# Optimization experiments

Measured on AMD Instinct MI355X. Metric: run time of the kernel, lower is better.

## Reference

```python
import jax, jax.numpy as jnp
import numpy as np

N0, N1, N2, N3 = 600000, 100000, 20000, 4096
E0, E1, E2 = 1500000, 200000, 40960
D_IN, D_H, D_OUT = 100, 256, 47


def setup_inputs() -> dict:
    key = jax.random.key(0)
    ks = jax.random.split(key, 16)
    inp = {
        "x": jax.random.normal(ks[0], (N0, D_IN), jnp.float32),
        "ei0_src": jax.random.randint(ks[1], (E0,), 0, N0, jnp.int32),
        "ei0_dst": jax.random.randint(ks[2], (E0,), 0, N1, jnp.int32),
        "ei1_src": jax.random.randint(ks[3], (E1,), 0, N1, jnp.int32),
        "ei1_dst": jax.random.randint(ks[4], (E1,), 0, N2, jnp.int32),
        "ei2_src": jax.random.randint(ks[5], (E2,), 0, N2, jnp.int32),
        "ei2_dst": jax.random.randint(ks[6], (E2,), 0, N3, jnp.int32),
        "Wl0": jax.random.normal(ks[7], (D_IN, D_H), jnp.float32) * 0.1,
        "Wr0": jax.random.normal(ks[8], (D_IN, D_H), jnp.float32) * 0.1,
        "b0": jnp.zeros((D_H,), jnp.float32),
        "Wl1": jax.random.normal(ks[9], (D_H, D_H), jnp.float32) * 0.06,
        "Wr1": jax.random.normal(ks[10], (D_H, D_H), jnp.float32) * 0.06,
        "b1": jnp.zeros((D_H,), jnp.float32),
        "Wl2": jax.random.normal(ks[11], (D_H, D_OUT), jnp.float32) * 0.06,
        "Wr2": jax.random.normal(ks[12], (D_H, D_OUT), jnp.float32) * 0.06,
        "b2": jnp.zeros((D_OUT,), jnp.float32),
    }
    return inp


def _sage_layer(x_src, x_tgt, src, dst, n_tgt, Wl, Wr, b):
    # PyG SAGEConv (mean aggr): out = lin_l(mean_{j in N(i)} x_j) + lin_r(x_i)
    msgs = x_src[src]                                   # [E, d] gather
    s = jax.ops.segment_sum(msgs, dst, num_segments=n_tgt)
    cnt = jax.ops.segment_sum(jnp.ones((src.shape[0],), x_src.dtype), dst,
                              num_segments=n_tgt)[:, None]
    mean = s / jnp.maximum(cnt, 1.0)
    return mean @ Wl + x_tgt @ Wr + b


def reference(x, ei0_src, ei0_dst, ei1_src, ei1_dst, ei2_src, ei2_dst,
              Wl0, Wr0, b0, Wl1, Wr1, b1, Wl2, Wr2, b2):
    h = _sage_layer(x, x[:N1], ei0_src, ei0_dst, N1, Wl0, Wr0, b0)
    h = jax.nn.relu(h)  # dropout is identity in eval mode
    h = _sage_layer(h, h[:N2], ei1_src, ei1_dst, N2, Wl1, Wr1, b1)
    h = jax.nn.relu(h)
    h = _sage_layer(h, h[:N3], ei2_src, ei2_dst, N3, Wl2, Wr2, b2)
    return jax.nn.log_softmax(h, axis=-1)
```

## Files before the change

kernel.cpp:

```cpp
#include <hip/hip_runtime.h>

#define NN0 600000
#define NN1 100000
#define NN2 20000
#define NN3 4096
#define EE0 1500000
#define EE1 200000
#define EE2 40960
#define DIN 100
#define DH  256
#define DOUT 47
#define NTOT (NN1 + NN2 + NN3)

#define RNG 16384
#define CH0 32768
#define NC0 46
#define R0  7
#define CH1 16384
#define NC1 13
#define R1  2
#define CH2 8192
#define NC2 5
#define R2  1
#define HL0 (NC0 * R0)
#define HL1 (NC1 * R1)
#define HL2 (NC2 * R2)
#define HLT (HL0 + HL1 + HL2)
#define NGMAX 46

#define NB0 98
#define NB1 20
#define NB2 4
#define NBT 122

#define HB0 5860
#define HB1 782
#define HB2 160
#define HBE (HB0 + HB1 + HB2)
#define PACKBLK 108
#define CONVBLK 3072

typedef unsigned int uint;
typedef unsigned short ushort;
typedef __attribute__((ext_vector_type(8))) short bhalf8;
typedef __attribute__((ext_vector_type(4))) float f32x4;

union U16B {
    uint2  u2[2];
    uint4  u4;
    bhalf8 s8;
    ushort us[8];
};

__device__ __forceinline__ ushort f2bf(float f) {
    uint u = __float_as_uint(f);
    uint r = (u + 0x7FFFu + ((u >> 16) & 1u)) >> 16;
    return (ushort)r;
}
__device__ __forceinline__ float bf2f(uint bits16) {
    return __uint_as_float(bits16 << 16);
}

__global__ __launch_bounds__(256)
void hist_lds(const int* __restrict__ e0d, const int* __restrict__ e1d,
              const int* __restrict__ e2d, int* __restrict__ cntp,
              int* __restrict__ pos0, int* __restrict__ pos1,
              int* __restrict__ pos2) {
    __shared__ int lcnt[RNG];
    int b = blockIdx.x, tid = threadIdx.x;
    const int* dstp; int E, CH, c, r, nbase, layerN;
    int* pos;
    if (b < HL0) {
        dstp = e0d; E = EE0; CH = CH0; c = b / R0; r = b % R0;
        nbase = 0; layerN = NN1; pos = pos0;
    } else if (b < HL0 + HL1) {
        int bb = b - HL0;
        dstp = e1d; E = EE1; CH = CH1; c = bb / R1; r = bb % R1;
        nbase = NN1; layerN = NN2; pos = pos1;
    } else {
        int bb = b - HL0 - HL1;
        dstp = e2d; E = EE2; CH = CH2; c = bb; r = 0;
        nbase = NN1 + NN2; layerN = NN3; pos = pos2;
    }
    for (int i = tid; i < RNG; i += 256) lcnt[i] = 0;
    __syncthreads();
    int rbase = r * RNG;
    long long ebase = (long long)c * CH;
    for (int i = tid; i < CH; i += 256) {
        int e = (int)(ebase + i);
        if (e < E) {
            int d = dstp[e];
            unsigned li = (unsigned)(d - rbase);
            if (li < RNG) pos[e] = atomicAdd(&lcnt[li], 1);
        }
    }
    __syncthreads();
    for (int i = tid; i < RNG; i += 256) {
        int node = rbase + i;
        if (node < layerN)
            cntp[(size_t)c * NTOT + nbase + node] = lcnt[i];
    }
}

__device__ __forceinline__ void pack_one(const float* B, int K, int N, int NB,
                                         ushort* out, int bid, int l) {
    int kstep = bid / NB;
    int c = bid % NB;
    U16B v;
    #pragma unroll
    for (int j = 0; j < 8; ++j) {
        int k = kstep * 32 + ((l >> 4) << 3) + j;
        int col = (c << 4) | (l & 15);
        float f = (k < K && col < N) ? B[(size_t)k * N + col] : 0.0f;
        v.us[j] = f2bf(f);
    }
    *reinterpret_cast<bhalf8*>(out + ((size_t)bid * 64 + l) * 8) = v.s8;
}

__global__ __launch_bounds__(256)
void conv_pack(const float* __restrict__ x, ushort* __restrict__ xb, long long n4,
               const float* __restrict__ Wl0, const float* __restrict__ Wr0,
               const float* __restrict__ Wl1, const float* __restrict__ Wr1,
               const float* __restrict__ Wl2, const float* __restrict__ Wr2,
               ushort* Bp0l, ushort* Bp0r, ushort* Bp1l, ushort* Bp1r,
               ushort* Bp2l, ushort* Bp2r) {
    int b = blockIdx.x;
    int tid = threadIdx.x;
    if (b < CONVBLK) {
        for (long long t = (long long)b * 256 + tid; t < n4;
             t += (long long)CONVBLK * 256) {
            float4 v = *reinterpret_cast<const float4*>(x + t * 4);
            uint2 o;
            o.x = (uint)f2bf(v.x) | ((uint)f2bf(v.y) << 16);
            o.y = (uint)f2bf(v.z) | ((uint)f2bf(v.w) << 16);
            *reinterpret_cast<uint2*>(xb + t * 4) = o;
        }
    } else {
        int bid = (b - CONVBLK) * 4 + (tid >> 6);
        int l = tid & 63;
        if (bid < 64)       pack_one(Wl0, DIN, DH,  16, Bp0l, bid,       l);
        else if (bid < 128) pack_one(Wr0, DIN, DH,  16, Bp0r, bid - 64,  l);
        else if (bid < 256) pack_one(Wl1, DH,  DH,  16, Bp1l, bid - 128, l);
        else if (bid < 384) pack_one(Wr1, DH,  DH,  16, Bp1r, bid - 256, l);
        else if (bid < 408) pack_one(Wl2, DH,  DOUT, 3, Bp2l, bid - 384, l);
        else                pack_one(Wr2, DH,  DOUT, 3, Bp2r, bid - 408, l);
    }
}

__global__ __launch_bounds__(256)
void combine_parts(int* __restrict__ cntp, int* __restrict__ cntAll) {
    int i = blockIdx.x * 256 + threadIdx.x;
    if (i >= NTOT) return;
    int ng = (i < NN1) ? NC0 : (i < NN1 + NN2) ? NC1 : NC2;
    int run = 0;
    for (int g = 0; g < ng; ++g) {
        size_t idx = (size_t)g * NTOT + i;
        int v = cntp[idx];
        cntp[idx] = run;
        run += v;
    }
    cntAll[i] = run;
}


__device__ __forceinline__ void layer_of(int b, int& lb, int& n, int& po, int& cb) {
    if (b < NB0)      { lb = b;        n = NN1; po = 0;         cb = 0; }
    else if (b < NB0 + NB1) { lb = b - NB0;  n = NN2; po = NB0; cb = NN1; }
    else              { lb = b - NB0 - NB1; n = NN3; po = NB0 + NB1; cb = NN1 + NN2; }
}

__global__ void scan1f(const int* __restrict__ cntAll, int* __restrict__ part) {
    int lb, n, po, cb;
    layer_of(blockIdx.x, lb, n, po, cb);
    __shared__ int s[256];
    int base = lb * 1024;
    int sum = 0;
    for (int i = threadIdx.x; i < 1024; i += 256) {
        int idx = base + i;
        sum += (idx < n) ? cntAll[cb + idx] : 0;
    }
    s[threadIdx.x] = sum;
    __syncthreads();
    for (int off = 128; off; off >>= 1) {
        if (threadIdx.x < off) s[threadIdx.x] += s[threadIdx.x + off];
        __syncthreads();
    }
    if (threadIdx.x == 0) part[po + lb] = s[0];
}

__global__ void scan2f(int* part) {
    __shared__ int s[128];
    int t = threadIdx.x;
    int seg = (t < NB0) ? 0 : (t < NB0 + NB1) ? 1 : (t < NBT) ? 2 : 3;
    int v = (t < NBT) ? part[t] : 0;
    s[t] = v;
    __syncthreads();
    for (int off = 1; off < 128; off <<= 1) {
        int add = 0;
        if (t >= off) {
            int u = t - off;
            int segu = (u < NB0) ? 0 : (u < NB0 + NB1) ? 1 : (u < NBT) ? 2 : 3;
            if (segu == seg) add = s[u];
        }
        __syncthreads();
        s[t] += add;
        __syncthreads();
    }
    if (t < NBT) part[t] = s[t] - v;
}

__global__ void scan3f(const int* __restrict__ cntAll, const int* __restrict__ part,
                       int* __restrict__ rp0, int* __restrict__ rp1,
                       int* __restrict__ rp2) {
    int lb, n, po, cb;
    layer_of(blockIdx.x, lb, n, po, cb);
    int* row_ptr;
    if (cb == 0)        row_ptr = rp0;
    else if (cb == NN1) row_ptr = rp1;
    else                row_ptr = rp2;

    __shared__ int s[256];
    int base = lb * 1024;
    int v[4];
    int sum = 0;
    #pragma unroll
    for (int j = 0; j < 4; ++j) {
        int idx = base + threadIdx.x * 4 + j;
        v[j] = (idx < n) ? cntAll[cb + idx] : 0;
        sum += v[j];
    }
    s[threadIdx.x] = sum;
    __syncthreads();
    for (int off = 1; off < 256; off <<= 1) {
        int t = (threadIdx.x >= off) ? s[threadIdx.x - off] : 0;
        __syncthreads();
        s[threadIdx.x] += t;
        __syncthreads();
    }
    int off0 = part[po + lb] + s[threadIdx.x] - sum;
    #pragma unroll
    for (int j = 0; j < 4; ++j) {
        int idx = base + threadIdx.x * 4 + j;
        if (idx < n) {
            row_ptr[idx] = off0;
            off0 += v[j];
            if (idx == n - 1) row_ptr[n] = off0;
        }
    }
}

__global__ __launch_bounds__(256)
void place_all(const int* __restrict__ e0s, const int* __restrict__ e0d,
               const int* __restrict__ e1s, const int* __restrict__ e1d,
               const int* __restrict__ e2s, const int* __restrict__ e2d,
               const int* __restrict__ pos0, const int* __restrict__ pos1,
               const int* __restrict__ pos2, const int* __restrict__ cntp,
               const int* __restrict__ rp0, const int* __restrict__ rp1,
               const int* __restrict__ rp2,
               int* __restrict__ eidx0, int* __restrict__ eidx1,
               int* __restrict__ eidx2) {
    int b = blockIdx.x;
    int tid = threadIdx.x;
    if (b < HB0) {
        int e = b * 256 + tid;
        if (e < EE0) {
            int d = e0d[e];
            int g = e >> 15;
            int p = rp0[d] + cntp[(size_t)g * NTOT + d] + pos0[e];
            eidx0[p] = e0s[e];
        }
    } else if (b < HB0 + HB1) {
        int e = (b - HB0) * 256 + tid;
        if (e < EE1) {
            int d = e1d[e];
            int g = e >> 14;
            int p = rp1[d] + cntp[(size_t)g * NTOT + NN1 + d] + pos1[e];
            eidx1[p] = e1s[e];
        }
    } else {
        int e = (b - HB0 - HB1) * 256 + tid;
        if (e < EE2) {
            int d = e2d[e];
            int g = e >> 13;
            int p = rp2[d] + cntp[(size_t)g * NTOT + NN1 + NN2 + d] + pos2[e];
            eidx2[p] = e2s[e];
        }
    }
}


__global__ __launch_bounds__(256)
void agg100_b(const ushort* __restrict__ xb, const int* __restrict__ rp,
              const int* __restrict__ eidx, ushort* __restrict__ out, int nNodes) {
    int node = blockIdx.x * 4 + (threadIdx.x >> 6);
    if (node >= nNodes) return;
    int l = threadIdx.x & 63;
    bool act = l < 50;
    int beg = rp[node], end = rp[node + 1];
    float a0 = 0.f, a1 = 0.f;
    int j = beg;
    for (; j + 3 < end; j += 4) {
        int s0 = eidx[j], s1 = eidx[j + 1], s2 = eidx[j + 2], s3 = eidx[j + 3];
        if (act) {
            uint v0 = *reinterpret_cast<const uint*>(xb + (size_t)s0 * DIN + l * 2);
            uint v1 = *reinterpret_cast<const uint*>(xb + (size_t)s1 * DIN + l * 2);
            uint v2 = *reinterpret_cast<const uint*>(xb + (size_t)s2 * DIN + l * 2);
            uint v3 = *reinterpret_cast<const uint*>(xb + (size_t)s3 * DIN + l * 2);
            a0 += bf2f(v0 & 0xffffu) + bf2f(v1 & 0xffffu) + bf2f(v2 & 0xffffu) + bf2f(v3 & 0xffffu);
            a1 += bf2f(v0 >> 16) + bf2f(v1 >> 16) + bf2f(v2 >> 16) + bf2f(v3 >> 16);
        }
    }
    for (; j < end; ++j) {
        int s0 = eidx[j];
        if (act) {
            uint v0 = *reinterpret_cast<const uint*>(xb + (size_t)s0 * DIN + l * 2);
            a0 += bf2f(v0 & 0xffffu);
            a1 += bf2f(v0 >> 16);
        }
    }
    float inv = 1.0f / fmaxf((float)(end - beg), 1.0f);
    if (act) {
        uint o = (uint)f2bf(a0 * inv) | ((uint)f2bf(a1 * inv) << 16);
        *reinterpret_cast<uint*>(out + (size_t)node * DIN + l * 2) = o;
    }
}

__global__ __launch_bounds__(256)
void agg100_f(const float* __restrict__ x, const int* __restrict__ rp,
              const int* __restrict__ eidx, ushort* __restrict__ out, int nNodes) {
    int node = blockIdx.x * 4 + (threadIdx.x >> 6);
    if (node >= nNodes) return;
    int l = threadIdx.x & 63;
    bool act = l < 50;
    int beg = rp[node], end = rp[node + 1];
    float a0 = 0.f, a1 = 0.f;
    int j = beg;
    for (; j + 1 < end; j += 2) {
        int s0 = eidx[j], s1 = eidx[j + 1];
        if (act) {
            float2 v0 = *reinterpret_cast<const float2*>(x + (size_t)s0 * DIN + l * 2);
            float2 v1 = *reinterpret_cast<const float2*>(x + (size_t)s1 * DIN + l * 2);
            a0 += v0.x + v1.x;
            a1 += v0.y + v1.y;
        }
    }
    if (j < end) {
        int s0 = eidx[j];
        if (act) {
            float2 v0 = *reinterpret_cast<const float2*>(x + (size_t)s0 * DIN + l * 2);
            a0 += v0.x; a1 += v0.y;
        }
    }
    float inv = 1.0f / fmaxf((float)(end - beg), 1.0f);
    if (act) {
        uint o = (uint)f2bf(a0 * inv) | ((uint)f2bf(a1 * inv) << 16);
        *reinterpret_cast<uint*>(out + (size_t)node * DIN + l * 2) = o;
    }
}

__global__ __launch_bounds__(256)
void agg256_b(const ushort* __restrict__ h, const int* __restrict__ rp,
              const int* __restrict__ eidx, ushort* __restrict__ out, int nNodes) {
    int node = blockIdx.x * 4 + (threadIdx.x >> 6);
    if (node >= nNodes) return;
    int l = threadIdx.x & 63;
    int beg = rp[node], end = rp[node + 1];
    float a0 = 0.f, a1 = 0.f, a2 = 0.f, a3 = 0.f;
    int j = beg;
    for (; j + 3 < end; j += 4) {
        int s0 = eidx[j], s1 = eidx[j + 1], s2 = eidx[j + 2], s3 = eidx[j + 3];
        uint2 v0 = *reinterpret_cast<const uint2*>(h + (size_t)s0 * DH + l * 4);
        uint2 v1 = *reinterpret_cast<const uint2*>(h + (size_t)s1 * DH + l * 4);
        uint2 v2 = *reinterpret_cast<const uint2*>(h + (size_t)s2 * DH + l * 4);
        uint2 v3 = *reinterpret_cast<const uint2*>(h + (size_t)s3 * DH + l * 4);
        a0 += bf2f(v0.x & 0xffffu) + bf2f(v1.x & 0xffffu) + bf2f(v2.x & 0xffffu) + bf2f(v3.x & 0xffffu);
        a1 += bf2f(v0.x >> 16)     + bf2f(v1.x >> 16)     + bf2f(v2.x >> 16)     + bf2f(v3.x >> 16);
        a2 += bf2f(v0.y & 0xffffu) + bf2f(v1.y & 0xffffu) + bf2f(v2.y & 0xffffu) + bf2f(v3.y & 0xffffu);
        a3 += bf2f(v0.y >> 16)     + bf2f(v1.y >> 16)     + bf2f(v2.y >> 16)     + bf2f(v3.y >> 16);
    }
    for (; j < end; ++j) {
        int s0 = eidx[j];
        uint2 v0 = *reinterpret_cast<const uint2*>(h + (size_t)s0 * DH + l * 4);
        a0 += bf2f(v0.x & 0xffffu);
        a1 += bf2f(v0.x >> 16);
        a2 += bf2f(v0.y & 0xffffu);
        a3 += bf2f(v0.y >> 16);
    }
    float inv = 1.0f / fmaxf((float)(end - beg), 1.0f);
    uint2 o;
    o.x = (uint)f2bf(a0 * inv) | ((uint)f2bf(a1 * inv) << 16);
    o.y = (uint)f2bf(a2 * inv) | ((uint)f2bf(a3 * inv) << 16);
    *reinterpret_cast<uint2*>(out + (size_t)node * DH + l * 4) = o;
}

template <int RELU, int OUTBF>
__global__ __launch_bounds__(256)
void gemm_dual(const ushort* __restrict__ A1, int K1, int S1, int str1,
               const ushort* __restrict__ A2, int K2, int S2, int str2,
               const ushort* __restrict__ B1p, const ushort* __restrict__ B2p,
               const float* __restrict__ bias, void* __restrict__ Cv,
               int M, int N, int NB, int NBW, int Cstride) {
    __shared__ ushort At[2][2048];

    const int tid = threadIdx.x;
    const int w = tid >> 6;
    const int l = tid & 63;
    const int m0 = blockIdx.x * 64;
    const int S = S1 + S2;

    f32x4 acc[4][4];
    #pragma unroll
    for (int m = 0; m < 4; ++m)
        #pragma unroll
        for (int i = 0; i < 4; ++i)
            acc[m][i] = f32x4{0.f, 0.f, 0.f, 0.f};

    auto stage = [&](int s, int buf) {
        const ushort* A; int str, Keff, ks;
        if (s < S1) { A = A1; str = str1; Keff = K1; ks = s; }
        else        { A = A2; str = str2; Keff = K2; ks = s - S1; }
        int r  = tid >> 2;
        int kc = tid & 3;
        int row = m0 + r;
        int k = ks * 32 + (kc << 3);
        U16B v;
        v.u4.x = v.u4.y = v.u4.z = v.u4.w = 0u;
        if (row < M && k < Keff) {
            const ushort* p = A + (size_t)row * str + k;
            v.u2[0] = *reinterpret_cast<const uint2*>(p);
            v.u2[1] = *reinterpret_cast<const uint2*>(p + 4);
            if (k + 8 > Keff) {
                #pragma unroll
                for (int j = 0; j < 8; ++j)
                    if (k + j >= Keff) v.us[j] = 0;
            }
        }
        int slot = ((r >> 4) << 6) | (r & 15) | (kc << 4);
        *reinterpret_cast<bhalf8*>(&At[buf][slot * 8]) = v.s8;
    };

    stage(0, 0);
    __syncthreads();

    for (int s = 0; s < S; ++s) {
        int buf = s & 1;
        if (s + 1 < S) stage(s + 1, buf ^ 1);

        const ushort* Bp; int ks;
        if (s < S1) { Bp = B1p; ks = s; }
        else        { Bp = B2p; ks = s - S1; }

        bhalf8 a[4];
        #pragma unroll
        for (int m = 0; m < 4; ++m)
            a[m] = *reinterpret_cast<bhalf8*>(&At[buf][((m << 6) | l) * 8]);

        #pragma unroll
        for (int i = 0; i < 4; ++i) {
            if (i < NBW) {
                int c = w * NBW + i;
                if (c < NB) {
                    bhalf8 b = *reinterpret_cast<const bhalf8*>(
                        Bp + ((size_t)(ks * NB + c) * 64 + l) * 8);
                    #pragma unroll
                    for (int m = 0; m < 4; ++m)
                        acc[m][i] = __builtin_amdgcn_mfma_f32_16x16x32_bf16(
                            a[m], b, acc[m][i], 0, 0, 0);
                }
            }
        }
        __syncthreads();
    }

    #pragma unroll
    for (int i = 0; i < 4; ++i) {
        if (i >= NBW) continue;
        int c = w * NBW + i;
        if (c >= NB) continue;
        int col = (c << 4) | (l & 15);
        if (col >= N) continue;
        float bb = bias[col];
        #pragma unroll
        for (int m = 0; m < 4; ++m) {
            #pragma unroll
            for (int e = 0; e < 4; ++e) {
                int row = m0 + (m << 4) + ((l >> 4) << 2) + e;
                if (row < M) {
                    float v = acc[m][i][e] + bb;
                    if (RELU) v = fmaxf(v, 0.0f);
                    if (OUTBF)
                        ((ushort*)Cv)[(size_t)row * Cstride + col] = f2bf(v);
                    else
                        ((float*)Cv)[(size_t)row * Cstride + col] = v;
                }
            }
        }
    }
}

__global__ void log_softmax_47(const float* __restrict__ z, float* __restrict__ out) {
    int row = blockIdx.x;
    int lane = threadIdx.x;
    float v = (lane < DOUT) ? z[(size_t)row * DOUT + lane] : -INFINITY;
    float m = v;
    #pragma unroll
    for (int off = 32; off; off >>= 1) m = fmaxf(m, __shfl_xor(m, off));
    float e = (lane < DOUT) ? expf(v - m) : 0.0f;
    float s = e;
    #pragma unroll
    for (int off = 32; off; off >>= 1) s += __shfl_xor(s, off);
    if (lane < DOUT) out[(size_t)row * DOUT + lane] = v - m - logf(s);
}

extern "C" void kernel_launch(void* const* d_in, const int* in_sizes, int n_in,
                              void* d_out, int out_size, void* d_ws, size_t ws_size,
                              hipStream_t stream) {
    const float* x   = (const float*)d_in[0];
    const int* e0s   = (const int*)d_in[1];
    const int* e0d   = (const int*)d_in[2];
    const int* e1s   = (const int*)d_in[3];
    const int* e1d   = (const int*)d_in[4];
    const int* e2s   = (const int*)d_in[5];
    const int* e2d   = (const int*)d_in[6];
    const float* Wl0 = (const float*)d_in[7];
    const float* Wr0 = (const float*)d_in[8];
    const float* b0  = (const float*)d_in[9];
    const float* Wl1 = (const float*)d_in[10];
    const float* Wr1 = (const float*)d_in[11];
    const float* b1  = (const float*)d_in[12];
    const float* Wl2 = (const float*)d_in[13];
    const float* Wr2 = (const float*)d_in[14];
    const float* b2  = (const float*)d_in[15];

    char* ws = (char*)d_ws;
    size_t off = 0;
    auto alloc = [&](size_t bytes) -> void* {
        void* p = ws + off;
        off += (bytes + 255) & ~(size_t)255;
        return p;
    };

    ushort* agg0b = (ushort*)alloc((size_t)NN1 * DIN * 2);
    ushort* h1    = (ushort*)alloc((size_t)NN1 * DH * 2);
    ushort* agg1b = (ushort*)alloc((size_t)NN2 * DH * 2);
    ushort* h2    = (ushort*)alloc((size_t)NN2 * DH * 2);
    ushort* agg2b = (ushort*)alloc((size_t)NN3 * DH * 2);
    float*  z     = (float*)alloc((size_t)NN3 * DOUT * 4);

    ushort* Bp0l = (ushort*)alloc((size_t)4 * 16 * 64 * 8 * 2);
    ushort* Bp0r = (ushort*)alloc((size_t)4 * 16 * 64 * 8 * 2);
    ushort* Bp1l = (ushort*)alloc((size_t)8 * 16 * 64 * 8 * 2);
    ushort* Bp1r = (ushort*)alloc((size_t)8 * 16 * 64 * 8 * 2);
    ushort* Bp2l = (ushort*)alloc((size_t)8 * 3 * 64 * 8 * 2);
    ushort* Bp2r = (ushort*)alloc((size_t)8 * 3 * 64 * 8 * 2);

    int* cntp   = (int*)alloc((size_t)NGMAX * NTOT * 4);
    int* cntAll = (int*)alloc((size_t)NTOT * 4);
    int* pos0   = (int*)alloc((size_t)EE0 * 4);
    int* pos1   = (int*)alloc((size_t)EE1 * 4);
    int* pos2   = (int*)alloc((size_t)EE2 * 4);
    int* rp0    = (int*)alloc((size_t)(NN1 + 1) * 4);
    int* eidx0  = (int*)alloc((size_t)EE0 * 4);
    int* rp1    = (int*)alloc((size_t)(NN2 + 1) * 4);
    int* eidx1  = (int*)alloc((size_t)EE1 * 4);
    int* rp2    = (int*)alloc((size_t)(NN3 + 1) * 4);
    int* eidx2  = (int*)alloc((size_t)EE2 * 4);
    int* part   = (int*)alloc(256 * 4);

    size_t fullNeed = (size_t)NN0 * DIN * 2 + 4096;
    bool big = (ws_size - off) >= fullNeed;
    int xRows = big ? NN0 : NN1;
    ushort* xb = (ushort*)alloc((size_t)xRows * DIN * 2 + 256);

    hist_lds<<<HLT, 256, 0, stream>>>(e0d, e1d, e2d, cntp, pos0, pos1, pos2);

    {
        long long n4 = (long long)xRows * DIN / 4;
        conv_pack<<<CONVBLK + PACKBLK, 256, 0, stream>>>(
            x, xb, n4, Wl0, Wr0, Wl1, Wr1, Wl2, Wr2,
            Bp0l, Bp0r, Bp1l, Bp1r, Bp2l, Bp2r);
    }

    combine_parts<<<(NTOT + 255) / 256, 256, 0, stream>>>(cntp, cntAll);
    scan1f<<<NBT, 256, 0, stream>>>(cntAll, part);
    scan2f<<<1, 128, 0, stream>>>(part);
    scan3f<<<NBT, 256, 0, stream>>>(cntAll, part, rp0, rp1, rp2);

    place_all<<<HBE, 256, 0, stream>>>(e0s, e0d, e1s, e1d, e2s, e2d,
                                       pos0, pos1, pos2, cntp,
                                       rp0, rp1, rp2, eidx0, eidx1, eidx2);

    if (big)
        agg100_b<<<(NN1 + 3) / 4, 256, 0, stream>>>(xb, rp0, eidx0, agg0b, NN1);
    else
        agg100_f<<<(NN1 + 3) / 4, 256, 0, stream>>>(x, rp0, eidx0, agg0b, NN1);
    gemm_dual<1, 1><<<(NN1 + 63) / 64, 256, 0, stream>>>(
        agg0b, DIN, 4, DIN, xb, DIN, 4, DIN, Bp0l, Bp0r, b0, h1,
        NN1, DH, 16, 4, DH);

    agg256_b<<<(NN2 + 3) / 4, 256, 0, stream>>>(h1, rp1, eidx1, agg1b, NN2);
    gemm_dual<1, 1><<<(NN2 + 63) / 64, 256, 0, stream>>>(
        agg1b, DH, 8, DH, h1, DH, 8, DH, Bp1l, Bp1r, b1, h2,
        NN2, DH, 16, 4, DH);

    agg256_b<<<(NN3 + 3) / 4, 256, 0, stream>>>(h2, rp2, eidx2, agg2b, NN3);
    gemm_dual<0, 0><<<(NN3 + 63) / 64, 256, 0, stream>>>(
        agg2b, DH, 8, DH, h2, DH, 8, DH, Bp2l, Bp2r, b2, z,
        NN3, DOUT, 3, 1, DOUT);

    log_softmax_47<<<NN3, 64, 0, stream>>>(z, (float*)d_out);
}
```

Before: 495.0 us.

## Drop bf16 pre-conversion of x; gather fp32 directly and convert in GEMM staging

Removes the pass that converts the full 600k-row input feature matrix to bf16. The layer-0 aggregation now gathers fp32 rows directly, with a 4-way unrolled edge loop, and the dual GEMM converts the root-feature operand from fp32 to bf16 while staging tiles. Weight packing moves into its own small kernel, and the histogram kernel switches to 1024-thread blocks. This avoids a large streaming read and write of x, but each random gather now moves twice as many bytes per source row.

```diff
diff --git a/kernel.cpp b/kernel.cpp
--- a/kernel.cpp
+++ b/kernel.cpp
@@ -37,8 +37,6 @@
 #define HB1 782
 #define HB2 160
 #define HBE (HB0 + HB1 + HB2)
-#define PACKBLK 108
-#define CONVBLK 3072
 
 typedef unsigned int uint;
 typedef unsigned short ushort;
@@ -61,7 +59,7 @@
     return __uint_as_float(bits16 << 16);
 }
 
-__global__ __launch_bounds__(256)
+__global__ __launch_bounds__(1024)
 void hist_lds(const int* __restrict__ e0d, const int* __restrict__ e1d,
               const int* __restrict__ e2d, int* __restrict__ cntp,
               int* __restrict__ pos0, int* __restrict__ pos1,
@@ -82,11 +80,11 @@
         dstp = e2d; E = EE2; CH = CH2; c = bb; r = 0;
         nbase = NN1 + NN2; layerN = NN3; pos = pos2;
     }
-    for (int i = tid; i < RNG; i += 256) lcnt[i] = 0;
+    for (int i = tid; i < RNG; i += 1024) lcnt[i] = 0;
     __syncthreads();
     int rbase = r * RNG;
     long long ebase = (long long)c * CH;
-    for (int i = tid; i < CH; i += 256) {
+    for (int i = tid; i < CH; i += 1024) {
         int e = (int)(ebase + i);
         if (e < E) {
             int d = dstp[e];
@@ -95,7 +93,7 @@
         }
     }
     __syncthreads();
-    for (int i = tid; i < RNG; i += 256) {
+    for (int i = tid; i < RNG; i += 1024) {
         int node = rbase + i;
         if (node < layerN)
             cntp[(size_t)c * NTOT + nbase + node] = lcnt[i];
@@ -118,33 +116,19 @@
 }
 
 __global__ __launch_bounds__(256)
-void conv_pack(const float* __restrict__ x, ushort* __restrict__ xb, long long n4,
-               const float* __restrict__ Wl0, const float* __restrict__ Wr0,
-               const float* __restrict__ Wl1, const float* __restrict__ Wr1,
-               const float* __restrict__ Wl2, const float* __restrict__ Wr2,
-               ushort* Bp0l, ushort* Bp0r, ushort* Bp1l, ushort* Bp1r,
-               ushort* Bp2l, ushort* Bp2r) {
-    int b = blockIdx.x;
-    int tid = threadIdx.x;
-    if (b < CONVBLK) {
-        for (long long t = (long long)b * 256 + tid; t < n4;
-             t += (long long)CONVBLK * 256) {
-            float4 v = *reinterpret_cast<const float4*>(x + t * 4);
-            uint2 o;
-            o.x = (uint)f2bf(v.x) | ((uint)f2bf(v.y) << 16);
-            o.y = (uint)f2bf(v.z) | ((uint)f2bf(v.w) << 16);
-            *reinterpret_cast<uint2*>(xb + t * 4) = o;
-        }
-    } else {
-        int bid = (b - CONVBLK) * 4 + (tid >> 6);
-        int l = tid & 63;
-        if (bid < 64)       pack_one(Wl0, DIN, DH,  16, Bp0l, bid,       l);
-        else if (bid < 128) pack_one(Wr0, DIN, DH,  16, Bp0r, bid - 64,  l);
-        else if (bid < 256) pack_one(Wl1, DH,  DH,  16, Bp1l, bid - 128, l);
-        else if (bid < 384) pack_one(Wr1, DH,  DH,  16, Bp1r, bid - 256, l);
-        else if (bid < 408) pack_one(Wl2, DH,  DOUT, 3, Bp2l, bid - 384, l);
-        else                pack_one(Wr2, DH,  DOUT, 3, Bp2r, bid - 408, l);
-    }
+void pack_all(const float* __restrict__ Wl0, const float* __restrict__ Wr0,
+              const float* __restrict__ Wl1, const float* __restrict__ Wr1,
+              const float* __restrict__ Wl2, const float* __restrict__ Wr2,
+              ushort* Bp0l, ushort* Bp0r, ushort* Bp1l, ushort* Bp1r,
+              ushort* Bp2l, ushort* Bp2r) {
+    int bid = blockIdx.x * 4 + (threadIdx.x >> 6);
+    int l = threadIdx.x & 63;
+    if (bid < 64)       pack_one(Wl0, DIN, DH,  16, Bp0l, bid,       l);
+    else if (bid < 128) pack_one(Wr0, DIN, DH,  16, Bp0r, bid - 64,  l);
+    else if (bid < 256) pack_one(Wl1, DH,  DH,  16, Bp1l, bid - 128, l);
+    else if (bid < 384) pack_one(Wr1, DH,  DH,  16, Bp1r, bid - 256, l);
+    else if (bid < 408) pack_one(Wl2, DH,  DOUT, 3, Bp2l, bid - 384, l);
+    else if (bid < 432) pack_one(Wr2, DH,  DOUT, 3, Bp2r, bid - 408, l);
 }
 
 __global__ __launch_bounds__(256)
@@ -290,7 +274,7 @@
 
 
 __global__ __launch_bounds__(256)
-void agg100_b(const ushort* __restrict__ xb, const int* __restrict__ rp,
+void agg100_f(const float* __restrict__ x, const int* __restrict__ rp,
               const int* __restrict__ eidx, ushort* __restrict__ out, int nNodes) {
     int node = blockIdx.x * 4 + (threadIdx.x >> 6);
     if (node >= nNodes) return;
@@ -302,49 +286,15 @@
     for (; j + 3 < end; j += 4) {
         int s0 = eidx[j], s1 = eidx[j + 1], s2 = eidx[j + 2], s3 = eidx[j + 3];
         if (act) {
-            uint v0 = *reinterpret_cast<const uint*>(xb + (size_t)s0 * DIN + l * 2);
-            uint v1 = *reinterpret_cast<const uint*>(xb + (size_t)s1 * DIN + l * 2);
-            uint v2 = *reinterpret_cast<const uint*>(xb + (size_t)s2 * DIN + l * 2);
-            uint v3 = *reinterpret_cast<const uint*>(xb + (size_t)s3 * DIN + l * 2);
-            a0 += bf2f(v0 & 0xffffu) + bf2f(v1 & 0xffffu) + bf2f(v2 & 0xffffu) + bf2f(v3 & 0xffffu);
-            a1 += bf2f(v0 >> 16) + bf2f(v1 >> 16) + bf2f(v2 >> 16) + bf2f(v3 >> 16);
-        }
-    }
-    for (; j < end; ++j) {
-        int s0 = eidx[j];
-        if (act) {
-            uint v0 = *reinterpret_cast<const uint*>(xb + (size_t)s0 * DIN + l * 2);
-            a0 += bf2f(v0 & 0xffffu);
-            a1 += bf2f(v0 >> 16);
-        }
-    }
-    float inv = 1.0f / fmaxf((float)(end - beg), 1.0f);
-    if (act) {
-        uint o = (uint)f2bf(a0 * inv) | ((uint)f2bf(a1 * inv) << 16);
-        *reinterpret_cast<uint*>(out + (size_t)node * DIN + l * 2) = o;
-    }
-}
-
-__global__ __launch_bounds__(256)
-void agg100_f(const float* __restrict__ x, const int* __restrict__ rp,
-              const int* __restrict__ eidx, ushort* __restrict__ out, int nNodes) {
-    int node = blockIdx.x * 4 + (threadIdx.x >> 6);
-    if (node >= nNodes) return;
-    int l = threadIdx.x & 63;
-    bool act = l < 50;
-    int beg = rp[node], end = rp[node + 1];
-    float a0 = 0.f, a1 = 0.f;
-    int j = beg;
-    for (; j + 1 < end; j += 2) {
-        int s0 = eidx[j], s1 = eidx[j + 1];
-        if (act) {
             float2 v0 = *reinterpret_cast<const float2*>(x + (size_t)s0 * DIN + l * 2);
             float2 v1 = *reinterpret_cast<const float2*>(x + (size_t)s1 * DIN + l * 2);
-            a0 += v0.x + v1.x;
-            a1 += v0.y + v1.y;
-        }
-    }
-    if (j < end) {
+            float2 v2 = *reinterpret_cast<const float2*>(x + (size_t)s2 * DIN + l * 2);
+            float2 v3 = *reinterpret_cast<const float2*>(x + (size_t)s3 * DIN + l * 2);
+            a0 += v0.x + v1.x + v2.x + v3.x;
+            a1 += v0.y + v1.y + v2.y + v3.y;
+        }
+    }
+    for (; j < end; ++j) {
         int s0 = eidx[j];
         if (act) {
             float2 v0 = *reinterpret_cast<const float2*>(x + (size_t)s0 * DIN + l * 2);
@@ -393,10 +343,10 @@
     *reinterpret_cast<uint2*>(out + (size_t)node * DH + l * 4) = o;
 }
 
-template <int RELU, int OUTBF>
+template <int RELU, int OUTBF, int A2F32>
 __global__ __launch_bounds__(256)
 void gemm_dual(const ushort* __restrict__ A1, int K1, int S1, int str1,
-               const ushort* __restrict__ A2, int K2, int S2, int str2,
+               const void* __restrict__ A2, int K2, int S2, int str2,
                const ushort* __restrict__ B1p, const ushort* __restrict__ B2p,
                const float* __restrict__ bias, void* __restrict__ Cv,
                int M, int N, int NB, int NBW, int Cstride) {
@@ -416,23 +366,45 @@
             acc[m][i] = f32x4{0.f, 0.f, 0.f, 0.f};
 
     auto stage = [&](int s, int buf) {
-        const ushort* A; int str, Keff, ks;
-        if (s < S1) { A = A1; str = str1; Keff = K1; ks = s; }
-        else        { A = A2; str = str2; Keff = K2; ks = s - S1; }
         int r  = tid >> 2;
         int kc = tid & 3;
         int row = m0 + r;
-        int k = ks * 32 + (kc << 3);
         U16B v;
         v.u4.x = v.u4.y = v.u4.z = v.u4.w = 0u;
-        if (row < M && k < Keff) {
-            const ushort* p = A + (size_t)row * str + k;
-            v.u2[0] = *reinterpret_cast<const uint2*>(p);
-            v.u2[1] = *reinterpret_cast<const uint2*>(p + 4);
-            if (k + 8 > Keff) {
-                #pragma unroll
-                for (int j = 0; j < 8; ++j)
-                    if (k + j >= Keff) v.us[j] = 0;
+        if (s < S1) {
+            int k = s * 32 + (kc << 3);
+            if (row < M && k < K1) {
+                const ushort* p = A1 + (size_t)row * str1 + k;
+                v.u2[0] = *reinterpret_cast<const uint2*>(p);
+                v.u2[1] = *reinterpret_cast<const uint2*>(p + 4);
+                if (k + 8 > K1) {
+                    #pragma unroll
+                    for (int j = 0; j < 8; ++j)
+                        if (k + j >= K1) v.us[j] = 0;
+                }
+            }
+        } else {
+            int ks = s - S1;
+            int k = ks * 32 + (kc << 3);
+            if (row < M && k < K2) {
+                if (A2F32) {
+                    const float* p = (const float*)A2 + (size_t)row * str2 + k;
+                    float4 f0 = *reinterpret_cast<const float4*>(p);
+                    float4 f1 = *reinterpret_cast<const float4*>(p + 4);
+                    v.us[0] = f2bf(f0.x); v.us[1] = f2bf(f0.y);
+                    v.us[2] = f2bf(f0.z); v.us[3] = f2bf(f0.w);
+                    v.us[4] = f2bf(f1.x); v.us[5] = f2bf(f1.y);
+                    v.us[6] = f2bf(f1.z); v.us[7] = f2bf(f1.w);
+                } else {
+                    const ushort* p = (const ushort*)A2 + (size_t)row * str2 + k;
+                    v.u2[0] = *reinterpret_cast<const uint2*>(p);
+                    v.u2[1] = *reinterpret_cast<const uint2*>(p + 4);
+                }
+                if (k + 8 > K2) {
+                    #pragma unroll
+                    for (int j = 0; j < 8; ++j)
+                        if (k + j >= K2) v.us[j] = 0;
+                }
             }
         }
         int slot = ((r >> 4) << 6) | (r & 15) | (kc << 4);
@@ -567,19 +539,9 @@
     int* eidx2  = (int*)alloc((size_t)EE2 * 4);
     int* part   = (int*)alloc(256 * 4);
 
-    size_t fullNeed = (size_t)NN0 * DIN * 2 + 4096;
-    bool big = (ws_size - off) >= fullNeed;
-    int xRows = big ? NN0 : NN1;
-    ushort* xb = (ushort*)alloc((size_t)xRows * DIN * 2 + 256);
-
-    hist_lds<<<HLT, 256, 0, stream>>>(e0d, e1d, e2d, cntp, pos0, pos1, pos2);
-
-    {
-        long long n4 = (long long)xRows * DIN / 4;
-        conv_pack<<<CONVBLK + PACKBLK, 256, 0, stream>>>(
-            x, xb, n4, Wl0, Wr0, Wl1, Wr1, Wl2, Wr2,
-            Bp0l, Bp0r, Bp1l, Bp1r, Bp2l, Bp2r);
-    }
+    hist_lds<<<HLT, 1024, 0, stream>>>(e0d, e1d, e2d, cntp, pos0, pos1, pos2);
+    pack_all<<<108, 256, 0, stream>>>(Wl0, Wr0, Wl1, Wr1, Wl2, Wr2,
+                                      Bp0l, Bp0r, Bp1l, Bp1r, Bp2l, Bp2r);
 
     combine_parts<<<(NTOT + 255) / 256, 256, 0, stream>>>(cntp, cntAll);
     scan1f<<<NBT, 256, 0, stream>>>(cntAll, part);
@@ -590,22 +552,19 @@
                                        pos0, pos1, pos2, cntp,
                                        rp0, rp1, rp2, eidx0, eidx1, eidx2);
 
-    if (big)
-        agg100_b<<<(NN1 + 3) / 4, 256, 0, stream>>>(xb, rp0, eidx0, agg0b, NN1);
-    else
-        agg100_f<<<(NN1 + 3) / 4, 256, 0, stream>>>(x, rp0, eidx0, agg0b, NN1);
-    gemm_dual<1, 1><<<(NN1 + 63) / 64, 256, 0, stream>>>(
-        agg0b, DIN, 4, DIN, xb, DIN, 4, DIN, Bp0l, Bp0r, b0, h1,
+    agg100_f<<<(NN1 + 3) / 4, 256, 0, stream>>>(x, rp0, eidx0, agg0b, NN1);
+    gemm_dual<1, 1, 1><<<(NN1 + 63) / 64, 256, 0, stream>>>(
+        agg0b, DIN, 4, DIN, (const void*)x, DIN, 4, DIN, Bp0l, Bp0r, b0, h1,
         NN1, DH, 16, 4, DH);
 
     agg256_b<<<(NN2 + 3) / 4, 256, 0, stream>>>(h1, rp1, eidx1, agg1b, NN2);
-    gemm_dual<1, 1><<<(NN2 + 63) / 64, 256, 0, stream>>>(
-        agg1b, DH, 8, DH, h1, DH, 8, DH, Bp1l, Bp1r, b1, h2,
+    gemm_dual<1, 1, 0><<<(NN2 + 63) / 64, 256, 0, stream>>>(
+        agg1b, DH, 8, DH, (const void*)h1, DH, 8, DH, Bp1l, Bp1r, b1, h2,
         NN2, DH, 16, 4, DH);
 
     agg256_b<<<(NN3 + 3) / 4, 256, 0, stream>>>(h2, rp2, eidx2, agg2b, NN3);
-    gemm_dual<0, 0><<<(NN3 + 63) / 64, 256, 0, stream>>>(
-        agg2b, DH, 8, DH, h2, DH, 8, DH, Bp2l, Bp2r, b2, z,
+    gemm_dual<0, 0, 0><<<(NN3 + 63) / 64, 256, 0, stream>>>(
+        agg2b, DH, 8, DH, (const void*)h2, DH, 8, DH, Bp2l, Bp2r, b2, z,
         NN3, DOUT, 3, 1, DOUT);
 
     log_softmax_47<<<NN3, 64, 0, stream>>>(z, (float*)d_out);
```

New measurement: 413.8 us. 1.2x faster.
